# Kernel tuning notes

Measured on AMD Instinct MI355X. Metric: run time of the kernel, lower is better.

## Reference

```python
import jax, jax.numpy as jnp
import numpy as np

B, N, D_MODEL, H = 2, 2048, 1024, 16
HD = D_MODEL // H  # head_dim = 64

def setup_inputs() -> dict:
    key = jax.random.key(0)
    ks = jax.random.split(key, 5)
    x = jax.random.normal(ks[0], (B, N, D_MODEL), dtype=jnp.float32)
    scale = 0.02
    # Linear weights stored as [in, out] (torch does x @ W.T with W [out,in]; equivalent math)
    Wq = jax.random.normal(ks[1], (D_MODEL, D_MODEL), dtype=jnp.float32) * scale
    Wk = jax.random.normal(ks[2], (D_MODEL, D_MODEL), dtype=jnp.float32) * scale
    Wv = jax.random.normal(ks[3], (D_MODEL, D_MODEL), dtype=jnp.float32) * scale
    Wo = jax.random.normal(ks[4], (D_MODEL, D_MODEL), dtype=jnp.float32) * scale
    return {"x": x, "Wq": Wq, "Wk": Wk, "Wv": Wv, "Wo": Wo}

def reference(x, Wq, Wk, Wv, Wo):
    b, n, _ = x.shape
    # QKV projections (no bias; qkv_bias=False)
    q = (x @ Wq).reshape(b, n, H, HD)
    k = (x @ Wk).reshape(b, n, H, HD)
    v = (x @ Wv).reshape(b, n, H, HD)
    # scores [b, h, q, k]
    scores = jnp.einsum('bqhd,bkhd->bhqk', q, k) / jnp.sqrt(jnp.float32(HD))
    causal = jnp.triu(jnp.ones((n, n), dtype=bool), k=1)  # True above diagonal -> masked
    scores = jnp.where(causal, -jnp.inf, scores)
    attn = jax.nn.softmax(scores, axis=-1)  # dropout p=0.0 -> identity
    ctx = jnp.einsum('bhqk,bkhd->bqhd', attn, v).reshape(b, n, D_MODEL)
    return ctx @ Wo
```

## Files before the change

### kernel.cpp

```cpp
#include <hip/hip_runtime.h>
#include <math.h>

#define D_MODEL 1024
#define NHEAD 16
#define HD 64
#define SEQ 2048
#define BATCH 2
#define MTOT (BATCH * SEQ)

typedef __attribute__((ext_vector_type(8))) short bf16x8;
typedef __attribute__((ext_vector_type(4))) float f32x4;

__device__ __forceinline__ unsigned short f2bf(float f) {
    unsigned int u = __float_as_uint(f);
    u += 0x7FFF + ((u >> 16) & 1);
    return (unsigned short)(u >> 16);
}

__device__ __forceinline__ unsigned int pk2bf(float a, float b) {
    unsigned int r;
    asm("v_cvt_pk_bf16_f32 %0, %1, %2" : "=v"(r) : "v"(a), "v"(b));
    return r;
}

__device__ __forceinline__ void async16(unsigned short* lds, const unsigned short* g) {
    __builtin_amdgcn_global_load_lds(
        (const __attribute__((address_space(1))) unsigned int*)g,
        (__attribute__((address_space(3))) unsigned int*)lds, 16, 0, 0);
}

__device__ __forceinline__ void BAR() {
    asm volatile("" ::: "memory");
    __builtin_amdgcn_s_barrier();
    asm volatile("" ::: "memory");
}

__global__ __launch_bounds__(256) void prep(const float* __restrict__ x,
                                            unsigned short* __restrict__ xb,
                                            const float* __restrict__ W0,
                                            const float* __restrict__ W1,
                                            const float* __restrict__ W2,
                                            const float* __restrict__ W3,
                                            unsigned short* __restrict__ Wt) {
    const int bid = blockIdx.x;
    const int tid = threadIdx.x;
    if (bid < 4096) {
        const int i = (bid * 256 + tid) * 4;
        float4 v = *(const float4*)(x + i);
        uint2 pk;
        pk.x = pk2bf(v.x, v.y);
        pk.y = pk2bf(v.z, v.w);
        *(uint2*)(xb + i) = pk;
    } else {
        __shared__ float T[32][33];
        const int t = bid - 4096;
        const int z = t >> 10, rem = t & 1023;
        const int n0 = (rem & 31) * 32, k0 = (rem >> 5) * 32;
        const float* W = (z == 0) ? W0 : (z == 1) ? W1 : (z == 2) ? W2 : W3;
        unsigned short* out = Wt + (size_t)z * D_MODEL * D_MODEL;
        const int tx = tid & 31, ty = tid >> 5;
#pragma unroll
        for (int i = 0; i < 4; ++i)
            T[ty + 8 * i][tx] = W[(size_t)(k0 + ty + 8 * i) * D_MODEL + n0 + tx];
        __syncthreads();
#pragma unroll
        for (int i = 0; i < 4; ++i)
            out[(size_t)(n0 + ty + 8 * i) * D_MODEL + k0 + tx] = f2bf(T[tx][ty + 8 * i]);
    }
}

__global__ __launch_bounds__(512, 2) void qkv_mfma(const unsigned short* __restrict__ A,
                                                   const unsigned short* __restrict__ Wt,
                                                   unsigned short* __restrict__ q,
                                                   unsigned short* __restrict__ k,
                                                   unsigned short* __restrict__ vt) {
    __shared__ unsigned short SM[57344];
    const int tid = threadIdx.x;
    const int wave = tid >> 6, lane = tid & 63;
    const int quad = lane >> 4, l16 = lane & 15;
    const int wm = wave >> 2, wn = wave & 3;

    const int bid = blockIdx.x;
    const int swz = (bid & 7) * 32 + (bid >> 3);
    const int by = swz >> 4, bx = swz & 15;
    const int m0 = by * 256;
    const int c0 = bx * 192;
    const unsigned short* Bz = Wt;

    const unsigned short* aptr[2];
    const unsigned short* bptr[2];
#pragma unroll
    for (int j = 0; j < 2; ++j) {
        const int s = j * 512 + tid;
        const int r = s >> 2;
        const int cg = (s & 3) ^ ((r + (r >> 2)) & 3);
        aptr[j] = A + (size_t)(m0 + r) * D_MODEL + cg * 8;
        const int rb = (r < 192) ? r : 191;
        bptr[j] = Bz + (size_t)(c0 + rb) * D_MODEL + cg * 8;
    }
    const int ldsA0 = (wave * 64) * 8, ldsA1 = (512 + wave * 64) * 8;
    const int ldsB0 = (wave * 64) * 8, ldsB1 = (512 + wave * 64) * 8;

    const int key = (l16 + (l16 >> 2)) & 3;
    const int chunk = quad ^ key;
    int aoff[8], boff[3];
#pragma unroll
    for (int mt = 0; mt < 8; ++mt)
        aoff[mt] = ((wm * 128 + mt * 16 + l16) * 4 + chunk) * 8;
#pragma unroll
    for (int nt = 0; nt < 3; ++nt)
        boff[nt] = ((wn * 48 + nt * 16 + l16) * 4 + chunk) * 8;

    f32x4 acc[8][3];
#pragma unroll
    for (int mt = 0; mt < 8; ++mt)
#pragma unroll
        for (int nt = 0; nt < 3; ++nt)
            acc[mt][nt] = (f32x4){0.f, 0.f, 0.f, 0.f};

    auto stageA = [&](int d, int ks, int T) {
        const int base = d * 28672 + ks * 8192;
        async16(SM + base + ldsA0, aptr[0] + T * 64 + ks * 32);
        async16(SM + base + ldsA1, aptr[1] + T * 64 + ks * 32);
    };
    auto stageB = [&](int d, int ks, int T) {
        const int base = d * 28672 + 16384 + ks * 6144;
        async16(SM + base + ldsB0, bptr[0] + T * 64 + ks * 32);
        if (wave < 4)
            async16(SM + base + ldsB1, bptr[1] + T * 64 + ks * 32);
    };
    auto dsA = [&](bf16x8* af, int mh, int d, int ks) {
        const int base = d * 28672 + ks * 8192;
#pragma unroll
        for (int i = 0; i < 4; ++i)
            af[i] = *(const bf16x8*)&SM[base + aoff[mh * 4 + i]];
    };
    auto dsB = [&](bf16x8* bf, int d, int ks) {
        const int base = d * 28672 + 16384 + ks * 6144;
#pragma unroll
        for (int i = 0; i < 3; ++i)
            bf[i] = *(const bf16x8*)&SM[base + boff[i]];
    };
    auto mfma12 = [&](bf16x8* af, bf16x8* bf, int mh) {
        __builtin_amdgcn_s_setprio(1);
#pragma unroll
        for (int i = 0; i < 4; ++i)
#pragma unroll
            for (int nt = 0; nt < 3; ++nt)
                acc[mh * 4 + i][nt] = __builtin_amdgcn_mfma_f32_16x16x32_bf16(
                    af[i], bf[nt], acc[mh * 4 + i][nt], 0, 0, 0);
        __builtin_amdgcn_s_setprio(0);
    };
    auto waitc = [&](bool nx) {
        if (nx) {
            if (wave < 4) asm volatile("s_waitcnt vmcnt(4)" ::: "memory");
            else          asm volatile("s_waitcnt vmcnt(3)" ::: "memory");
        } else {
            asm volatile("s_waitcnt vmcnt(0)" ::: "memory");
        }
    };

    stageA(0, 0, 0);
    stageB(0, 0, 0);
    stageA(0, 1, 0);
    stageB(0, 1, 0);
    waitc(true);
    BAR();

    const int NT = D_MODEL / 64;
    for (int T = 0; T < NT; ++T) {
        const int d = T & 1, dn = d ^ 1;
        const bool nx = (T + 1 < NT);
        bf16x8 af[4], bf[3];
        dsA(af, 0, d, 0);
        dsB(bf, d, 0);
        if (nx) stageA(dn, 0, T + 1);
        __builtin_amdgcn_sched_barrier(0);
        BAR();
        mfma12(af, bf, 0);
        BAR();
        dsA(af, 1, d, 0);
        if (nx) stageB(dn, 0, T + 1);
        waitc(nx);
        __builtin_amdgcn_sched_barrier(0);
        BAR();
        mfma12(af, bf, 1);
        BAR();
        dsA(af, 0, d, 1);
        dsB(bf, d, 1);
        if (nx) stageA(dn, 1, T + 1);
        __builtin_amdgcn_sched_barrier(0);
        BAR();
        mfma12(af, bf, 0);
        BAR();
        dsA(af, 1, d, 1);
        if (nx) stageB(dn, 1, T + 1);
        waitc(nx);
        __builtin_amdgcn_sched_barrier(0);
        BAR();
        mfma12(af, bf, 1);
        BAR();
    }

    __syncthreads();
    const int bb = m0 >> 11, tok0 = m0 & (SEQ - 1);
#pragma unroll 1
    for (int G = 0; G < 3; ++G) {
        if (G) __syncthreads();
        const int gcol = c0 + G * 64;
        const int zg = gcol >> 10;
        const int hg = (gcol >> 6) & 15;
        if (zg < 2) {
            const float sc = (zg == 0) ? 0.18033688011112042f : 1.0f;
            unsigned short* dst = (zg == 0) ? q : k;
#pragma unroll
            for (int nt = 0; nt < 3; ++nt) {
                const int colb = wn * 48 + nt * 16;
                if ((colb >> 6) == G) {
                    const int cl = colb - G * 64 + l16;
#pragma unroll
                    for (int mt = 0; mt < 8; ++mt)
#pragma unroll
                        for (int reg = 0; reg < 4; ++reg) {
                            const int rr = wm * 128 + mt * 16 + quad * 4 + reg;
                            SM[rr * 64 + cl] = f2bf(acc[mt][nt][reg] * sc);
                        }
                }
            }
            __syncthreads();
#pragma unroll
            for (int it = 0; it < 4; ++it) {
                const int g = it * 512 + tid;
                const int r = g >> 3, c8 = g & 7;
                uint4 val = *(const uint4*)&SM[r * 64 + c8 * 8];
                *(uint4*)(dst + (((size_t)bb * NHEAD + hg) * SEQ + tok0 + r) * HD +
                          c8 * 8) = val;
            }
        } else {
#pragma unroll
            for (int nt = 0; nt < 3; ++nt) {
                const int colb = wn * 48 + nt * 16;
                if ((colb >> 6) == G) {
                    const int dl = colb - G * 64 + l16;
#pragma unroll
                    for (int mt = 0; mt < 8; ++mt) {
                        const int m = wm * 128 + mt * 16 + quad * 4;
                        uint2 w;
                        w.x = pk2bf(acc[mt][nt][0], acc[mt][nt][1]);
                        w.y = pk2bf(acc[mt][nt][2], acc[mt][nt][3]);
                        *(uint2*)&SM[dl * 264 + m] = w;
                    }
                }
            }
            __syncthreads();
#pragma unroll
            for (int it = 0; it < 4; ++it) {
                const int g = it * 512 + tid;
                const int dd = g >> 5, t8 = (g & 31) * 8;
                uint4 val = *(const uint4*)&SM[dd * 264 + t8];
                *(uint4*)(vt + (((size_t)bb * NHEAD + hg) * HD + dd) * SEQ + tok0 +
                          t8) = val;
            }
        }
    }
}

__global__ __launch_bounds__(256) void gemm_out(const unsigned short* __restrict__ A,
                                                const unsigned short* __restrict__ Bw,
                                                float* __restrict__ outf) {
    __shared__ unsigned short SM[12288];
    const int tid = threadIdx.x;
    const int m0 = blockIdx.y * 64, n0 = blockIdx.x * 128;
    const int wave = tid >> 6, lane = tid & 63;
    const int quad = lane >> 4, l16 = lane & 15;
    const int wm = wave & 1, wn = wave >> 1;

    f32x4 acc[2][4];
#pragma unroll
    for (int mt = 0; mt < 2; ++mt)
#pragma unroll
        for (int nt = 0; nt < 4; ++nt)
            acc[mt][nt] = (f32x4){0.f, 0.f, 0.f, 0.f};

    for (int k0 = 0; k0 < D_MODEL; k0 += 64) {
        __syncthreads();
#pragma unroll
        for (int i = 0; i < 2; ++i) {
            const int c = i * 256 + tid;
            const int r = c >> 3, cc = (c & 7) * 8;
            const int cbase = i * 256 + wave * 64;
            async16(SM + cbase * 8, A + (size_t)(m0 + r) * D_MODEL + k0 + cc);
        }
#pragma unroll
        for (int i = 0; i < 4; ++i) {
            const int c = i * 256 + tid;
            const int r = c >> 3, cc = (c & 7) * 8;
            const int cbase = i * 256 + wave * 64;
            async16(SM + 4096 + cbase * 8, Bw + (size_t)(n0 + r) * D_MODEL + k0 + cc);
        }
        __syncthreads();
#pragma unroll
        for (int ks = 0; ks < 2; ++ks) {
            bf16x8 af[2], bfr[4];
#pragma unroll
            for (int mt = 0; mt < 2; ++mt)
                af[mt] = *(const bf16x8*)&SM[(wm * 32 + mt * 16 + l16) * 64 + ks * 32 + quad * 8];
#pragma unroll
            for (int nt = 0; nt < 4; ++nt)
                bfr[nt] = *(const bf16x8*)&SM[4096 + (wn * 64 + nt * 16 + l16) * 64 + ks * 32 + quad * 8];
#pragma unroll
            for (int mt = 0; mt < 2; ++mt)
#pragma unroll
                for (int nt = 0; nt < 4; ++nt)
                    acc[mt][nt] = __builtin_amdgcn_mfma_f32_16x16x32_bf16(
                        af[mt], bfr[nt], acc[mt][nt], 0, 0, 0);
        }
    }

#pragma unroll
    for (int mt = 0; mt < 2; ++mt)
#pragma unroll
        for (int nt = 0; nt < 4; ++nt)
#pragma unroll
            for (int reg = 0; reg < 4; ++reg) {
                const int m = m0 + wm * 32 + mt * 16 + quad * 4 + reg;
                const int n = n0 + wn * 64 + nt * 16 + l16;
                outf[(size_t)m * D_MODEL + n] = acc[mt][nt][reg];
            }
}

__global__ __launch_bounds__(256, 2) void attn_mfma(const unsigned short* __restrict__ Q,
                                                    const unsigned short* __restrict__ K,
                                                    const unsigned short* __restrict__ VT,
                                                    unsigned short* __restrict__ ctx) {
    __shared__ float CMB[8832];
    const int tid = threadIdx.x;
    const int wave = tid >> 6, lane = tid & 63;
    const int quad = lane >> 4, l16 = lane & 15;
    const int h = blockIdx.x, b = blockIdx.z;
    const int p = 31 - (int)blockIdx.y;
    const int row0 = p * 64;
    const unsigned short* Qp = Q + ((size_t)b * NHEAD + h) * SEQ * HD;
    const unsigned short* Kp = K + ((size_t)b * NHEAD + h) * SEQ * HD;
    const unsigned short* Vp = VT + ((size_t)b * NHEAD + h) * HD * SEQ;
    unsigned short* Pw = (unsigned short*)CMB + wave * 4096;
    const int sw8 = l16 & 7;

    bf16x8 bQ[4][2];
#pragma unroll
    for (int f = 0; f < 4; ++f)
#pragma unroll
        for (int ks = 0; ks < 2; ++ks)
            bQ[f][ks] = *(const bf16x8*)(Qp +
                (size_t)(row0 + f * 16 + l16) * HD + ks * 32 + quad * 8);

    f32x4 o[4][4];
    float ps[4] = {0.f, 0.f, 0.f, 0.f};
#pragma unroll
    for (int nt = 0; nt < 4; ++nt)
#pragma unroll
        for (int f = 0; f < 4; ++f)
            o[nt][f] = (f32x4){0.f, 0.f, 0.f, 0.f};

    for (int kt = wave; kt <= p; kt += 4) {
        bf16x8 aK[4][2];
#pragma unroll
        for (int mt = 0; mt < 4; ++mt)
#pragma unroll
            for (int ks = 0; ks < 2; ++ks)
                aK[mt][ks] = *(const bf16x8*)(Kp +
                    (size_t)(kt * 64 + mt * 16 + l16) * HD + ks * 32 + quad * 8);

        f32x4 sT[4][4];
        __builtin_amdgcn_s_setprio(1);
#pragma unroll
        for (int mt = 0; mt < 4; ++mt)
#pragma unroll
            for (int f = 0; f < 4; ++f) {
                sT[mt][f] = __builtin_amdgcn_mfma_f32_16x16x32_bf16(
                    aK[mt][0], bQ[f][0], (f32x4){0.f, 0.f, 0.f, 0.f}, 0, 0, 0);
                sT[mt][f] = __builtin_amdgcn_mfma_f32_16x16x32_bf16(
                    aK[mt][1], bQ[f][1], sT[mt][f], 0, 0, 0);
            }
        __builtin_amdgcn_s_setprio(0);

        bf16x8 aV[4][2];
#pragma unroll
        for (int nt = 0; nt < 4; ++nt)
#pragma unroll
            for (int ks = 0; ks < 2; ++ks)
                aV[nt][ks] = *(const bf16x8*)(Vp +
                    (size_t)(nt * 16 + l16) * SEQ + kt * 64 + ks * 32 + quad * 8);

        const bool diag = (kt == p);
#pragma unroll
        for (int mt = 0; mt < 4; ++mt)
#pragma unroll
            for (int f = 0; f < 4; ++f) {
                float pv[4];
#pragma unroll
                for (int reg = 0; reg < 4; ++reg)
                    pv[reg] = __builtin_amdgcn_exp2f(sT[mt][f][reg]);
                if (diag) {
                    const int kb = kt * 64 + mt * 16 + quad * 4;
                    const int qg = row0 + f * 16 + l16;
#pragma unroll
                    for (int reg = 0; reg < 4; ++reg)
                        pv[reg] = (kb + reg > qg) ? 0.f : pv[reg];
                }
                ps[f] += (pv[0] + pv[1]) + (pv[2] + pv[3]);
                uint2 w;
                w.x = pk2bf(pv[0], pv[1]);
                w.y = pk2bf(pv[2], pv[3]);
                const int gph = ((mt * 2 + (quad >> 1)) ^ sw8);
                *(uint2*)&Pw[(f * 16 + l16) * 64 + gph * 8 + (quad & 1) * 4] = w;
            }

        bf16x8 bP[4][2];
#pragma unroll
        for (int f = 0; f < 4; ++f)
#pragma unroll
            for (int ks = 0; ks < 2; ++ks)
                bP[f][ks] = *(const bf16x8*)&Pw[(f * 16 + l16) * 64 +
                                                ((ks * 4 + quad) ^ sw8) * 8];

        __builtin_amdgcn_s_setprio(1);
#pragma unroll
        for (int nt = 0; nt < 4; ++nt)
#pragma unroll
            for (int f = 0; f < 4; ++f) {
                o[nt][f] = __builtin_amdgcn_mfma_f32_16x16x32_bf16(
                    aV[nt][0], bP[f][0], o[nt][f], 0, 0, 0);
                o[nt][f] = __builtin_amdgcn_mfma_f32_16x16x32_bf16(
                    aV[nt][1], bP[f][1], o[nt][f], 0, 0, 0);
            }
        __builtin_amdgcn_s_setprio(0);
    }

#pragma unroll
    for (int f = 0; f < 4; ++f) {
        ps[f] += __shfl_xor(ps[f], 16);
        ps[f] += __shfl_xor(ps[f], 32);
    }

    __syncthreads();
    if (wave >= 2) {
        float* Rg = CMB + (wave - 2) * 4352;
#pragma unroll
        for (int nt = 0; nt < 4; ++nt)
#pragma unroll
            for (int f = 0; f < 4; ++f)
                *(f32x4*)&Rg[(f * 16 + l16) * 68 + nt * 16 + quad * 4] = o[nt][f];
        if (quad == 0)
#pragma unroll
            for (int f = 0; f < 4; ++f)
                CMB[8704 + (wave - 2) * 64 + f * 16 + l16] = ps[f];
    }
    __syncthreads();
    if (wave < 2) {
        float* Rg = CMB + wave * 4352;
#pragma unroll
        for (int nt = 0; nt < 4; ++nt)
#pragma unroll
            for (int f = 0; f < 4; ++f)
                o[nt][f] += *(const f32x4*)&Rg[(f * 16 + l16) * 68 + nt * 16 + quad * 4];
#pragma unroll
        for (int f = 0; f < 4; ++f)
            ps[f] += CMB[8704 + wave * 64 + f * 16 + l16];
    }
    __syncthreads();
    if (wave == 1) {
#pragma unroll
        for (int nt = 0; nt < 4; ++nt)
#pragma unroll
            for (int f = 0; f < 4; ++f)
                *(f32x4*)&CMB[(f * 16 + l16) * 68 + nt * 16 + quad * 4] = o[nt][f];
        if (quad == 0)
#pragma unroll
            for (int f = 0; f < 4; ++f)
                CMB[8704 + f * 16 + l16] = ps[f];
    }
    __syncthreads();
    if (wave == 0) {
#pragma unroll
        for (int nt = 0; nt < 4; ++nt)
#pragma unroll
            for (int f = 0; f < 4; ++f)
                o[nt][f] += *(const f32x4*)&CMB[(f * 16 + l16) * 68 + nt * 16 + quad * 4];
        float inv[4];
#pragma unroll
        for (int f = 0; f < 4; ++f)
            inv[f] = 1.f / (ps[f] + CMB[8704 + f * 16 + l16]);
#pragma unroll
        for (int nt = 0; nt < 4; ++nt)
#pragma unroll
            for (int f = 0; f < 4; ++f) {
                const int tok = row0 + f * 16 + l16;
                const int col = h * HD + nt * 16 + quad * 4;
                uint2 w;
                w.x = pk2bf(o[nt][f][0] * inv[f], o[nt][f][1] * inv[f]);
                w.y = pk2bf(o[nt][f][2] * inv[f], o[nt][f][3] * inv[f]);
                *(uint2*)(ctx + ((size_t)b * SEQ + tok) * D_MODEL + col) = w;
            }
    }
}

extern "C" void kernel_launch(void* const* d_in, const int* in_sizes, int n_in,
                              void* d_out, int out_size, void* d_ws, size_t ws_size,
                              hipStream_t stream) {
    const float* x  = (const float*)d_in[0];
    const float* Wq = (const float*)d_in[1];
    const float* Wk = (const float*)d_in[2];
    const float* Wv = (const float*)d_in[3];
    const float* Wo = (const float*)d_in[4];
    float* out = (float*)d_out;

    unsigned short* ws = (unsigned short*)d_ws;
    const size_t T = (size_t)MTOT * D_MODEL;
    unsigned short* xb  = ws;
    unsigned short* Wt  = ws + T;
    unsigned short* q   = ws + 2 * T;
    unsigned short* k   = ws + 3 * T;
    unsigned short* vt  = ws + 4 * T;
    unsigned short* ctx = ws + 5 * T;

    prep<<<dim3(8192), dim3(256), 0, stream>>>(x, xb, Wq, Wk, Wv, Wo, Wt);

    qkv_mfma<<<dim3(256), dim3(512), 0, stream>>>(xb, Wt, q, k, vt);

    attn_mfma<<<dim3(NHEAD, 32, BATCH), dim3(256), 0, stream>>>(q, k, vt, ctx);

    gemm_out<<<dim3(8, 64), dim3(256), 0, stream>>>(ctx, Wt + 3 * (size_t)D_MODEL * D_MODEL, out);
}
```

Before: 176.6 us.

## Halve QKV GEMM M-tile and pair causal query blocks per attention workgroup

The QKV projection GEMM M-tile drops from 256 to 128 rows, doubling the grid to 512 workgroups and shrinking LDS and accumulator usage. This aims to improve CU occupancy and load balance, at the cost of more B-tile reloads per output. The attention kernel now processes two query blocks per workgroup, pairing block y with block 31-y so every workgroup gets equal causal work. Its grid halves to 16 in y, trading fewer workgroups for balanced tails.

```diff
diff --git a/kernel.cpp b/kernel.cpp
--- a/kernel.cpp
+++ b/kernel.cpp
@@ -74,87 +74,90 @@
                                                    unsigned short* __restrict__ q,
                                                    unsigned short* __restrict__ k,
                                                    unsigned short* __restrict__ vt) {
-    __shared__ unsigned short SM[57344];
+    __shared__ unsigned short SM[40960];
     const int tid = threadIdx.x;
     const int wave = tid >> 6, lane = tid & 63;
     const int quad = lane >> 4, l16 = lane & 15;
     const int wm = wave >> 2, wn = wave & 3;
 
     const int bid = blockIdx.x;
-    const int swz = (bid & 7) * 32 + (bid >> 3);
+    const int swz = (bid & 7) * 64 + (bid >> 3);
     const int by = swz >> 4, bx = swz & 15;
-    const int m0 = by * 256;
+    const int m0 = by * 128;
     const int c0 = bx * 192;
     const unsigned short* Bz = Wt;
 
-    const unsigned short* aptr[2];
+    const unsigned short* aptr;
+    {
+        const int s = tid, r = s >> 2;
+        const int cg = (s & 3) ^ ((r + (r >> 2)) & 3);
+        aptr = A + (size_t)(m0 + r) * D_MODEL + cg * 8;
+    }
     const unsigned short* bptr[2];
 #pragma unroll
     for (int j = 0; j < 2; ++j) {
         const int s = j * 512 + tid;
         const int r = s >> 2;
         const int cg = (s & 3) ^ ((r + (r >> 2)) & 3);
-        aptr[j] = A + (size_t)(m0 + r) * D_MODEL + cg * 8;
         const int rb = (r < 192) ? r : 191;
         bptr[j] = Bz + (size_t)(c0 + rb) * D_MODEL + cg * 8;
     }
-    const int ldsA0 = (wave * 64) * 8, ldsA1 = (512 + wave * 64) * 8;
-    const int ldsB0 = (wave * 64) * 8, ldsB1 = (512 + wave * 64) * 8;
+    const int ldsA0 = wave * 512;
+    const int ldsB0 = wave * 512, ldsB1 = 4096 + wave * 512;
 
     const int key = (l16 + (l16 >> 2)) & 3;
     const int chunk = quad ^ key;
-    int aoff[8], boff[3];
-#pragma unroll
-    for (int mt = 0; mt < 8; ++mt)
-        aoff[mt] = ((wm * 128 + mt * 16 + l16) * 4 + chunk) * 8;
+    int aoff[4], boff[3];
+#pragma unroll
+    for (int mt = 0; mt < 4; ++mt)
+        aoff[mt] = ((wm * 64 + mt * 16 + l16) * 4 + chunk) * 8;
 #pragma unroll
     for (int nt = 0; nt < 3; ++nt)
         boff[nt] = ((wn * 48 + nt * 16 + l16) * 4 + chunk) * 8;
 
-    f32x4 acc[8][3];
-#pragma unroll
-    for (int mt = 0; mt < 8; ++mt)
+    f32x4 acc[4][3];
+#pragma unroll
+    for (int mt = 0; mt < 4; ++mt)
 #pragma unroll
         for (int nt = 0; nt < 3; ++nt)
             acc[mt][nt] = (f32x4){0.f, 0.f, 0.f, 0.f};
 
     auto stageA = [&](int d, int ks, int T) {
-        const int base = d * 28672 + ks * 8192;
-        async16(SM + base + ldsA0, aptr[0] + T * 64 + ks * 32);
-        async16(SM + base + ldsA1, aptr[1] + T * 64 + ks * 32);
+        const int base = d * 20480 + ks * 4096;
+        async16(SM + base + ldsA0, aptr + T * 64 + ks * 32);
     };
     auto stageB = [&](int d, int ks, int T) {
-        const int base = d * 28672 + 16384 + ks * 6144;
+        const int base = d * 20480 + 8192 + ks * 6144;
         async16(SM + base + ldsB0, bptr[0] + T * 64 + ks * 32);
         if (wave < 4)
             async16(SM + base + ldsB1, bptr[1] + T * 64 + ks * 32);
     };
     auto dsA = [&](bf16x8* af, int mh, int d, int ks) {
-        const int base = d * 28672 + ks * 8192;
-#pragma unroll
-        for (int i = 0; i < 4; ++i)
-            af[i] = *(const bf16x8*)&SM[base + aoff[mh * 4 + i]];
+        const int base = d * 20480 + ks * 4096;
+#pragma unroll
+        for (int i = 0; i < 2; ++i)
+            af[i] = *(const bf16x8*)&SM[base + aoff[mh * 2 + i]];
     };
     auto dsB = [&](bf16x8* bf, int d, int ks) {
-        const int base = d * 28672 + 16384 + ks * 6144;
+        const int base = d * 20480 + 8192 + ks * 6144;
 #pragma unroll
         for (int i = 0; i < 3; ++i)
             bf[i] = *(const bf16x8*)&SM[base + boff[i]];
     };
-    auto mfma12 = [&](bf16x8* af, bf16x8* bf, int mh) {
+    auto mfma6 = [&](bf16x8* af, bf16x8* bf, int mh) {
         __builtin_amdgcn_s_setprio(1);
 #pragma unroll
-        for (int i = 0; i < 4; ++i)
+        for (int i = 0; i < 2; ++i)
 #pragma unroll
             for (int nt = 0; nt < 3; ++nt)
-                acc[mh * 4 + i][nt] = __builtin_amdgcn_mfma_f32_16x16x32_bf16(
-                    af[i], bf[nt], acc[mh * 4 + i][nt], 0, 0, 0);
+                acc[mh * 2 + i][nt] = __builtin_amdgcn_mfma_f32_16x16x32_bf16(
+                    af[i], bf[nt], acc[mh * 2 + i][nt], 0, 0, 0);
         __builtin_amdgcn_s_setprio(0);
     };
     auto waitc = [&](bool nx) {
         if (nx) {
-            if (wave < 4) asm volatile("s_waitcnt vmcnt(4)" ::: "memory");
-            else          asm volatile("s_waitcnt vmcnt(3)" ::: "memory");
+            if (wave < 4) asm volatile("s_waitcnt vmcnt(3)" ::: "memory");
+            else          asm volatile("s_waitcnt vmcnt(2)" ::: "memory");
         } else {
             asm volatile("s_waitcnt vmcnt(0)" ::: "memory");
         }
@@ -171,34 +174,34 @@
     for (int T = 0; T < NT; ++T) {
         const int d = T & 1, dn = d ^ 1;
         const bool nx = (T + 1 < NT);
-        bf16x8 af[4], bf[3];
+        bf16x8 af[2], bf[3];
         dsA(af, 0, d, 0);
         dsB(bf, d, 0);
         if (nx) stageA(dn, 0, T + 1);
         __builtin_amdgcn_sched_barrier(0);
         BAR();
-        mfma12(af, bf, 0);
+        mfma6(af, bf, 0);
         BAR();
         dsA(af, 1, d, 0);
         if (nx) stageB(dn, 0, T + 1);
         waitc(nx);
         __builtin_amdgcn_sched_barrier(0);
         BAR();
-        mfma12(af, bf, 1);
+        mfma6(af, bf, 1);
         BAR();
         dsA(af, 0, d, 1);
         dsB(bf, d, 1);
         if (nx) stageA(dn, 1, T + 1);
         __builtin_amdgcn_sched_barrier(0);
         BAR();
-        mfma12(af, bf, 0);
+        mfma6(af, bf, 0);
         BAR();
         dsA(af, 1, d, 1);
         if (nx) stageB(dn, 1, T + 1);
         waitc(nx);
         __builtin_amdgcn_sched_barrier(0);
         BAR();
-        mfma12(af, bf, 1);
+        mfma6(af, bf, 1);
         BAR();
     }
 
@@ -219,17 +222,17 @@
                 if ((colb >> 6) == G) {
                     const int cl = colb - G * 64 + l16;
 #pragma unroll
-                    for (int mt = 0; mt < 8; ++mt)
+                    for (int mt = 0; mt < 4; ++mt)
 #pragma unroll
                         for (int reg = 0; reg < 4; ++reg) {
-                            const int rr = wm * 128 + mt * 16 + quad * 4 + reg;
+                            const int rr = wm * 64 + mt * 16 + quad * 4 + reg;
                             SM[rr * 64 + cl] = f2bf(acc[mt][nt][reg] * sc);
                         }
                 }
             }
             __syncthreads();
 #pragma unroll
-            for (int it = 0; it < 4; ++it) {
+            for (int it = 0; it < 2; ++it) {
                 const int g = it * 512 + tid;
                 const int r = g >> 3, c8 = g & 7;
                 uint4 val = *(const uint4*)&SM[r * 64 + c8 * 8];
@@ -243,21 +246,21 @@
                 if ((colb >> 6) == G) {
                     const int dl = colb - G * 64 + l16;
 #pragma unroll
-                    for (int mt = 0; mt < 8; ++mt) {
-                        const int m = wm * 128 + mt * 16 + quad * 4;
+                    for (int mt = 0; mt < 4; ++mt) {
+                        const int m = wm * 64 + mt * 16 + quad * 4;
                         uint2 w;
                         w.x = pk2bf(acc[mt][nt][0], acc[mt][nt][1]);
                         w.y = pk2bf(acc[mt][nt][2], acc[mt][nt][3]);
-                        *(uint2*)&SM[dl * 264 + m] = w;
+                        *(uint2*)&SM[dl * 136 + m] = w;
                     }
                 }
             }
             __syncthreads();
 #pragma unroll
-            for (int it = 0; it < 4; ++it) {
+            for (int it = 0; it < 2; ++it) {
                 const int g = it * 512 + tid;
-                const int dd = g >> 5, t8 = (g & 31) * 8;
-                uint4 val = *(const uint4*)&SM[dd * 264 + t8];
+                const int dd = g >> 4, t8 = (g & 15) * 8;
+                uint4 val = *(const uint4*)&SM[dd * 136 + t8];
                 *(uint4*)(vt + (((size_t)bb * NHEAD + hg) * HD + dd) * SEQ + tok0 +
                           t8) = val;
             }
@@ -338,170 +341,176 @@
     const int wave = tid >> 6, lane = tid & 63;
     const int quad = lane >> 4, l16 = lane & 15;
     const int h = blockIdx.x, b = blockIdx.z;
-    const int p = 31 - (int)blockIdx.y;
-    const int row0 = p * 64;
+    const int y = blockIdx.y;
     const unsigned short* Qp = Q + ((size_t)b * NHEAD + h) * SEQ * HD;
     const unsigned short* Kp = K + ((size_t)b * NHEAD + h) * SEQ * HD;
     const unsigned short* Vp = VT + ((size_t)b * NHEAD + h) * HD * SEQ;
     unsigned short* Pw = (unsigned short*)CMB + wave * 4096;
     const int sw8 = l16 & 7;
 
-    bf16x8 bQ[4][2];
-#pragma unroll
-    for (int f = 0; f < 4; ++f)
-#pragma unroll
-        for (int ks = 0; ks < 2; ++ks)
-            bQ[f][ks] = *(const bf16x8*)(Qp +
-                (size_t)(row0 + f * 16 + l16) * HD + ks * 32 + quad * 8);
-
-    f32x4 o[4][4];
-    float ps[4] = {0.f, 0.f, 0.f, 0.f};
-#pragma unroll
-    for (int nt = 0; nt < 4; ++nt)
+#pragma unroll 1
+    for (int half = 0; half < 2; ++half) {
+        const int p = half ? y : (31 - y);
+        const int row0 = p * 64;
+        if (half) __syncthreads();
+
+        bf16x8 bQ[4][2];
 #pragma unroll
         for (int f = 0; f < 4; ++f)
-            o[nt][f] = (f32x4){0.f, 0.f, 0.f, 0.f};
-
-    for (int kt = wave; kt <= p; kt += 4) {
-        bf16x8 aK[4][2];
-#pragma unroll
-        for (int mt = 0; mt < 4; ++mt)
 #pragma unroll
             for (int ks = 0; ks < 2; ++ks)
-                aK[mt][ks] = *(const bf16x8*)(Kp +
-                    (size_t)(kt * 64 + mt * 16 + l16) * HD + ks * 32 + quad * 8);
-
-        f32x4 sT[4][4];
-        __builtin_amdgcn_s_setprio(1);
-#pragma unroll
-        for (int mt = 0; mt < 4; ++mt)
-#pragma unroll
-            for (int f = 0; f < 4; ++f) {
-                sT[mt][f] = __builtin_amdgcn_mfma_f32_16x16x32_bf16(
-                    aK[mt][0], bQ[f][0], (f32x4){0.f, 0.f, 0.f, 0.f}, 0, 0, 0);
-                sT[mt][f] = __builtin_amdgcn_mfma_f32_16x16x32_bf16(
-                    aK[mt][1], bQ[f][1], sT[mt][f], 0, 0, 0);
-            }
-        __builtin_amdgcn_s_setprio(0);
-
-        bf16x8 aV[4][2];
+                bQ[f][ks] = *(const bf16x8*)(Qp +
+                    (size_t)(row0 + f * 16 + l16) * HD + ks * 32 + quad * 8);
+
+        f32x4 o[4][4];
+        float ps[4] = {0.f, 0.f, 0.f, 0.f};
 #pragma unroll
         for (int nt = 0; nt < 4; ++nt)
 #pragma unroll
-            for (int ks = 0; ks < 2; ++ks)
-                aV[nt][ks] = *(const bf16x8*)(Vp +
-                    (size_t)(nt * 16 + l16) * SEQ + kt * 64 + ks * 32 + quad * 8);
-
-        const bool diag = (kt == p);
-#pragma unroll
-        for (int mt = 0; mt < 4; ++mt)
-#pragma unroll
-            for (int f = 0; f < 4; ++f) {
-                float pv[4];
-#pragma unroll
-                for (int reg = 0; reg < 4; ++reg)
-                    pv[reg] = __builtin_amdgcn_exp2f(sT[mt][f][reg]);
-                if (diag) {
-                    const int kb = kt * 64 + mt * 16 + quad * 4;
-                    const int qg = row0 + f * 16 + l16;
+            for (int f = 0; f < 4; ++f)
+                o[nt][f] = (f32x4){0.f, 0.f, 0.f, 0.f};
+
+        for (int kt = wave; kt <= p; kt += 4) {
+            bf16x8 aK[4][2];
+#pragma unroll
+            for (int mt = 0; mt < 4; ++mt)
+#pragma unroll
+                for (int ks = 0; ks < 2; ++ks)
+                    aK[mt][ks] = *(const bf16x8*)(Kp +
+                        (size_t)(kt * 64 + mt * 16 + l16) * HD + ks * 32 + quad * 8);
+
+            f32x4 sT[4][4];
+            __builtin_amdgcn_s_setprio(1);
+#pragma unroll
+            for (int mt = 0; mt < 4; ++mt)
+#pragma unroll
+                for (int f = 0; f < 4; ++f) {
+                    sT[mt][f] = __builtin_amdgcn_mfma_f32_16x16x32_bf16(
+                        aK[mt][0], bQ[f][0], (f32x4){0.f, 0.f, 0.f, 0.f}, 0, 0, 0);
+                    sT[mt][f] = __builtin_amdgcn_mfma_f32_16x16x32_bf16(
+                        aK[mt][1], bQ[f][1], sT[mt][f], 0, 0, 0);
+                }
+            __builtin_amdgcn_s_setprio(0);
+
+            bf16x8 aV[4][2];
+#pragma unroll
+            for (int nt = 0; nt < 4; ++nt)
+#pragma unroll
+                for (int ks = 0; ks < 2; ++ks)
+                    aV[nt][ks] = *(const bf16x8*)(Vp +
+                        (size_t)(nt * 16 + l16) * SEQ + kt * 64 + ks * 32 + quad * 8);
+
+            const bool diag = (kt == p);
+#pragma unroll
+            for (int mt = 0; mt < 4; ++mt)
+#pragma unroll
+                for (int f = 0; f < 4; ++f) {
+                    float pv[4];
 #pragma unroll
                     for (int reg = 0; reg < 4; ++reg)
-                        pv[reg] = (kb + reg > qg) ? 0.f : pv[reg];
+                        pv[reg] = __builtin_amdgcn_exp2f(sT[mt][f][reg]);
+                    if (diag) {
+                        const int kb = kt * 64 + mt * 16 + quad * 4;
+                        const int qg = row0 + f * 16 + l16;
+#pragma unroll
+                        for (int reg = 0; reg < 4; ++reg)
+                            pv[reg] = (kb + reg > qg) ? 0.f : pv[reg];
+                    }
+                    ps[f] += (pv[0] + pv[1]) + (pv[2] + pv[3]);
+                    uint2 w;
+                    w.x = pk2bf(pv[0], pv[1]);
+                    w.y = pk2bf(pv[2], pv[3]);
+                    const int gph = ((mt * 2 + (quad >> 1)) ^ sw8);
+                    *(uint2*)&Pw[(f * 16 + l16) * 64 + gph * 8 + (quad & 1) * 4] = w;
                 }
-                ps[f] += (pv[0] + pv[1]) + (pv[2] + pv[3]);
-                uint2 w;
-                w.x = pk2bf(pv[0], pv[1]);
-                w.y = pk2bf(pv[2], pv[3]);
-                const int gph = ((mt * 2 + (quad >> 1)) ^ sw8);
-                *(uint2*)&Pw[(f * 16 + l16) * 64 + gph * 8 + (quad & 1) * 4] = w;
-            }
-
-        bf16x8 bP[4][2];
-#pragma unroll
-        for (int f = 0; f < 4; ++f)
-#pragma unroll
-            for (int ks = 0; ks < 2; ++ks)
-                bP[f][ks] = *(const bf16x8*)&Pw[(f * 16 + l16) * 64 +
-                                                ((ks * 4 + quad) ^ sw8) * 8];
-
-        __builtin_amdgcn_s_setprio(1);
-#pragma unroll
-        for (int nt = 0; nt < 4; ++nt)
-#pragma unroll
-            for (int f = 0; f < 4; ++f) {
-                o[nt][f] = __builtin_amdgcn_mfma_f32_16x16x32_bf16(
-                    aV[nt][0], bP[f][0], o[nt][f], 0, 0, 0);
-                o[nt][f] = __builtin_amdgcn_mfma_f32_16x16x32_bf16(
-                    aV[nt][1], bP[f][1], o[nt][f], 0, 0, 0);
-            }
-        __builtin_amdgcn_s_setprio(0);
-    }
-
-#pragma unroll
-    for (int f = 0; f < 4; ++f) {
-        ps[f] += __shfl_xor(ps[f], 16);
-        ps[f] += __shfl_xor(ps[f], 32);
-    }
-
-    __syncthreads();
-    if (wave >= 2) {
-        float* Rg = CMB + (wave - 2) * 4352;
-#pragma unroll
-        for (int nt = 0; nt < 4; ++nt)
+
+            bf16x8 bP[4][2];
 #pragma unroll
             for (int f = 0; f < 4; ++f)
-                *(f32x4*)&Rg[(f * 16 + l16) * 68 + nt * 16 + quad * 4] = o[nt][f];
-        if (quad == 0)
+#pragma unroll
+                for (int ks = 0; ks < 2; ++ks)
+                    bP[f][ks] = *(const bf16x8*)&Pw[(f * 16 + l16) * 64 +
+                                                    ((ks * 4 + quad) ^ sw8) * 8];
+
+            __builtin_amdgcn_s_setprio(1);
+#pragma unroll
+            for (int nt = 0; nt < 4; ++nt)
+#pragma unroll
+                for (int f = 0; f < 4; ++f) {
+                    o[nt][f] = __builtin_amdgcn_mfma_f32_16x16x32_bf16(
+                        aV[nt][0], bP[f][0], o[nt][f], 0, 0, 0);
+                    o[nt][f] = __builtin_amdgcn_mfma_f32_16x16x32_bf16(
+                        aV[nt][1], bP[f][1], o[nt][f], 0, 0, 0);
+                }
+            __builtin_amdgcn_s_setprio(0);
+        }
+
+#pragma unroll
+        for (int f = 0; f < 4; ++f) {
+            ps[f] += __shfl_xor(ps[f], 16);
+            ps[f] += __shfl_xor(ps[f], 32);
+        }
+
+        __syncthreads();
+        if (wave >= 2) {
+            float* Rg = CMB + (wave - 2) * 4352;
+#pragma unroll
+            for (int nt = 0; nt < 4; ++nt)
+#pragma unroll
+                for (int f = 0; f < 4; ++f)
+                    *(f32x4*)&Rg[(f * 16 + l16) * 68 + nt * 16 + quad * 4] = o[nt][f];
+            if (quad == 0)
+#pragma unroll
+                for (int f = 0; f < 4; ++f)
+                    CMB[8704 + (wave - 2) * 64 + f * 16 + l16] = ps[f];
+        }
+        __syncthreads();
+        if (wave < 2) {
+            float* Rg = CMB + wave * 4352;
+#pragma unroll
+            for (int nt = 0; nt < 4; ++nt)
+#pragma unroll
+                for (int f = 0; f < 4; ++f)
+                    o[nt][f] += *(const f32x4*)&Rg[(f * 16 + l16) * 68 + nt * 16 + quad * 4];
 #pragma unroll
             for (int f = 0; f < 4; ++f)
-                CMB[8704 + (wave - 2) * 64 + f * 16 + l16] = ps[f];
-    }
-    __syncthreads();
-    if (wave < 2) {
-        float* Rg = CMB + wave * 4352;
-#pragma unroll
-        for (int nt = 0; nt < 4; ++nt)
+                ps[f] += CMB[8704 + wave * 64 + f * 16 + l16];
+        }
+        __syncthreads();
+        if (wave == 1) {
+#pragma unroll
+            for (int nt = 0; nt < 4; ++nt)
+#pragma unroll
+                for (int f = 0; f < 4; ++f)
+                    *(f32x4*)&CMB[(f * 16 + l16) * 68 + nt * 16 + quad * 4] = o[nt][f];
+            if (quad == 0)
+#pragma unroll
+                for (int f = 0; f < 4; ++f)
+                    CMB[8704 + f * 16 + l16] = ps[f];
+        }
+        __syncthreads();
+        if (wave == 0) {
+#pragma unroll
+            for (int nt = 0; nt < 4; ++nt)
+#pragma unroll
+                for (int f = 0; f < 4; ++f)
+                    o[nt][f] += *(const f32x4*)&CMB[(f * 16 + l16) * 68 + nt * 16 + quad * 4];
+            float inv[4];
 #pragma unroll
             for (int f = 0; f < 4; ++f)
-                o[nt][f] += *(const f32x4*)&Rg[(f * 16 + l16) * 68 + nt * 16 + quad * 4];
-#pragma unroll
-        for (int f = 0; f < 4; ++f)
-            ps[f] += CMB[8704 + wave * 64 + f * 16 + l16];
-    }
-    __syncthreads();
-    if (wave == 1) {
-#pragma unroll
-        for (int nt = 0; nt < 4; ++nt)
-#pragma unroll
-            for (int f = 0; f < 4; ++f)
-                *(f32x4*)&CMB[(f * 16 + l16) * 68 + nt * 16 + quad * 4] = o[nt][f];
-        if (quad == 0)
-#pragma unroll
-            for (int f = 0; f < 4; ++f)
-                CMB[8704 + f * 16 + l16] = ps[f];
-    }
-    __syncthreads();
-    if (wave == 0) {
-#pragma unroll
-        for (int nt = 0; nt < 4; ++nt)
-#pragma unroll
-            for (int f = 0; f < 4; ++f)
-                o[nt][f] += *(const f32x4*)&CMB[(f * 16 + l16) * 68 + nt * 16 + quad * 4];
-        float inv[4];
-#pragma unroll
-        for (int f = 0; f < 4; ++f)
-            inv[f] = 1.f / (ps[f] + CMB[8704 + f * 16 + l16]);
-#pragma unroll
-        for (int nt = 0; nt < 4; ++nt)
-#pragma unroll
-            for (int f = 0; f < 4; ++f) {
-                const int tok = row0 + f * 16 + l16;
-                const int col = h * HD + nt * 16 + quad * 4;
-                uint2 w;
-                w.x = pk2bf(o[nt][f][0] * inv[f], o[nt][f][1] * inv[f]);
-                w.y = pk2bf(o[nt][f][2] * inv[f], o[nt][f][3] * inv[f]);
-                *(uint2*)(ctx + ((size_t)b * SEQ + tok) * D_MODEL + col) = w;
-            }
+                inv[f] = 1.f / (ps[f] + CMB[8704 + f * 16 + l16]);
+#pragma unroll
+            for (int nt = 0; nt < 4; ++nt)
+#pragma unroll
+                for (int f = 0; f < 4; ++f) {
+                    const int tok = row0 + f * 16 + l16;
+                    const int col = h * HD + nt * 16 + quad * 4;
+                    uint2 w;
+                    w.x = pk2bf(o[nt][f][0] * inv[f], o[nt][f][1] * inv[f]);
+                    w.y = pk2bf(o[nt][f][2] * inv[f], o[nt][f][3] * inv[f]);
+                    *(uint2*)(ctx + ((size_t)b * SEQ + tok) * D_MODEL + col) = w;
+                }
+        }
     }
 }
 
@@ -526,9 +535,9 @@
 
     prep<<<dim3(8192), dim3(256), 0, stream>>>(x, xb, Wq, Wk, Wv, Wo, Wt);
 
-    qkv_mfma<<<dim3(256), dim3(512), 0, stream>>>(xb, Wt, q, k, vt);
-
-    attn_mfma<<<dim3(NHEAD, 32, BATCH), dim3(256), 0, stream>>>(q, k, vt, ctx);
+    qkv_mfma<<<dim3(512), dim3(512), 0, stream>>>(xb, Wt, q, k, vt);
+
+    attn_mfma<<<dim3(NHEAD, 16, BATCH), dim3(256), 0, stream>>>(q, k, vt, ctx);
 
     gemm_out<<<dim3(8, 64), dim3(256), 0, stream>>>(ctx, Wt + 3 * (size_t)D_MODEL * D_MODEL, out);
 }
```

Result: no change. 174.2 us (-1.3%).
